# Optimization experiments

Hardware: AMD Instinct MI355X
Metric: run time of the kernel (lower is better)

The kernel has to match this reference:

```python
import jax, jax.numpy as jnp
import numpy as np

B = 1024      # graphs
NODES = 128   # nodes per graph (uniform -> batch_ptr = arange(B+1)*NODES)
IN = 64
HID = 256
OUT = 128
NBLK = 3
TAU = 0.25


def _ln(x, g, b):
    # LayerNorm over last dim, eps=1e-5 (torch default)
    mu = jnp.mean(x, axis=-1, keepdims=True)
    var = jnp.mean((x - mu) ** 2, axis=-1, keepdims=True)
    return (x - mu) / jnp.sqrt(var + 1e-5) * g + b


def setup_inputs() -> dict:
    key = jax.random.key(0)
    ks = jax.random.split(key, 4)
    sc = 0.05
    return {
        "H": jax.random.normal(ks[0], (B * NODES, IN), jnp.float32),
        "batch_ptr": jnp.arange(B + 1, dtype=jnp.int32) * NODES,
        # ResNetMLP params: stem Linear(IN->HID)+LN, NBLK residual blocks
        # Linear(HID->HID)+LN+ReLU, head Linear(HID->OUT)+LN (last_norm=True).
        "W_in": jax.random.normal(ks[1], (IN, HID), jnp.float32) * sc,
        "b_in": jnp.zeros((HID,), jnp.float32),
        "g_in": jnp.ones((HID,), jnp.float32),
        "beta_in": jnp.zeros((HID,), jnp.float32),
        "Wb": jax.random.normal(ks[2], (NBLK, HID, HID), jnp.float32) * sc,
        "bb": jnp.zeros((NBLK, HID), jnp.float32),
        "gb": jnp.ones((NBLK, HID), jnp.float32),
        "betab": jnp.zeros((NBLK, HID), jnp.float32),
        "W_out": jax.random.normal(ks[3], (HID, OUT), jnp.float32) * sc,
        "b_out": jnp.zeros((OUT,), jnp.float32),
        "g_out": jnp.ones((OUT,), jnp.float32),
        "beta_out": jnp.zeros((OUT,), jnp.float32),
    }


def reference(H, batch_ptr, W_in, b_in, g_in, beta_in, Wb, bb, gb, betab,
              W_out, b_out, g_out, beta_out):
    # ResNetMLP projection (dropout is identity in eval)
    x = jax.nn.relu(_ln(H @ W_in + b_in, g_in, beta_in))          # [N, HID]
    for k in range(NBLK):
        x = x + jax.nn.relu(_ln(x @ Wb[k] + bb[k], gb[k], betab[k]))
    z = _ln(x @ W_out + b_out, g_out, beta_out)                   # [N, OUT]

    # Uniform-size graphs: ragged per-graph loop vectorizes to [Bg, n, OUT]
    Bg = batch_ptr.shape[0] - 1
    n = H.shape[0] // Bg
    z3 = z.reshape(Bg, n, OUT)

    # s_i = mean_j ||z_i - z_j||_2 (includes j=i, distance 0)
    sq = jnp.sum(z3 * z3, axis=-1)                                # [Bg, n]
    d2 = sq[:, :, None] + sq[:, None, :] - 2.0 * jnp.einsum("bid,bjd->bij", z3, z3)
    d = jnp.sqrt(jnp.maximum(d2, 0.0) + 1e-12)                    # [Bg, n, n]
    s = jnp.mean(d, axis=-1)                                      # [Bg, n]

    w = jax.nn.softmax(s / TAU, axis=-1)                          # [Bg, n]
    v_loc = jnp.einsum("bi,bid->bd", w, z3)                       # [Bg, OUT]
    return v_loc, w
```

## Files before the change

kernel.cpp:

```cpp
#include <hip/hip_runtime.h>
#include <stdint.h>


typedef __attribute__((ext_vector_type(8))) short bf16x8;
typedef __attribute__((ext_vector_type(4))) float f32x4;

#define XB_STRIDE 264
#define YB_STRIDE 260
#define ZB_STRIDE 136
#define LDS_PAR   33280
#define LDS_TOTAL 36352

__device__ __forceinline__ unsigned int rne16(float f) {
  unsigned int u = __builtin_bit_cast(unsigned int, f);
  return u + 0x7fffu + ((u >> 16) & 1u);
}
__device__ __forceinline__ unsigned short f2bf(float f) {
  return (unsigned short)(rne16(f) >> 16);
}
__device__ __forceinline__ float bf2f(unsigned short h) {
  unsigned int u = ((unsigned int)h) << 16;
  return __builtin_bit_cast(float, u);
}
__device__ __forceinline__ f32x4 zero4() {
  f32x4 v; v.x = 0.f; v.y = 0.f; v.z = 0.f; v.w = 0.f; return v;
}
template <int CTRL>
__device__ __forceinline__ float dpp_add(float v) {
  int p = __builtin_amdgcn_update_dpp(0, __builtin_bit_cast(int, v),
                                      CTRL, 0xF, 0xF, true);
  return v + __builtin_bit_cast(float, p);
}
__device__ __forceinline__ float red16(float v) {
  v = dpp_add<0xB1>(v);
  v = dpp_add<0x4E>(v);
  v = dpp_add<0x141>(v);
  v = dpp_add<0x140>(v);
  return v;
}

__global__ void prep_weights(const float* __restrict__ Win, const float* __restrict__ Wb,
                             const float* __restrict__ Wout, unsigned short* __restrict__ ws) {
  int g = blockIdx.x * 256 + threadIdx.x;
  if (g >= 30720) return;
  const float* W; int N; int local;
  if (g < 2048) { W = Win; N = 256; local = g; }
  else if (g < 26624) {
    int i = g - 2048; int blk = i >> 13; local = i & 8191;
    W = Wb + blk * 65536; N = 256;
  } else { W = Wout; N = 128; local = g - 26624; }
  int f = local >> 6, lane = local & 63;
  int NTL = N >> 4;
  int kc = f / NTL, ntile = f - kc * NTL;
  int n = ntile * 16 + (lane & 15);
  int k0 = kc * 32 + (lane >> 4) * 8;
  unsigned short o[8];
#pragma unroll
  for (int e = 0; e < 8; ++e) o[e] = f2bf(W[(size_t)(k0 + e) * N + n]);
  *reinterpret_cast<uint4*>(ws + (size_t)g * 8) = *reinterpret_cast<uint4*>(o);
}

template <int KL, int N, int MODE>
__device__ __forceinline__ void layer(unsigned short* __restrict__ Xb,
                                      float* __restrict__ Yb, float* __restrict__ par,
                                      const unsigned short* __restrict__ Wf,
                                      int tid, int wave, int lane,
                                      const float* __restrict__ bias,
                                      const float* __restrict__ gam,
                                      const float* __restrict__ bet,
                                      float (&xprev)[16],
                                      unsigned short* __restrict__ Z, size_t rowglob) {
  constexpr int NT = N / 128;
  constexpr int NTL = N / 16;
  constexpr int KC = KL / 32;
  constexpr int J = N / 64;
  const int wc = wave;
  const int q = lane >> 4, l16 = lane & 15;
  const int colbase = wc * 16 * NT;
  const unsigned short* Wl = Wf + lane * 8;

  f32x4 acc[2][NT];
#pragma unroll
  for (int mt = 0; mt < 2; ++mt)
#pragma unroll
    for (int nt = 0; nt < NT; ++nt) acc[mt][nt] = zero4();

  bf16x8 bcur[NT];
#pragma unroll
  for (int nt = 0; nt < NT; ++nt)
    bcur[nt] = *reinterpret_cast<const bf16x8*>(Wl + (size_t)(wc * NT + nt) * 512);

  __syncthreads();
  for (int t = tid; t < 3 * N; t += 512) {
    float v = (t < N) ? bias[t] : (t < 2 * N) ? gam[t - N] : bet[t - 2 * N];
    par[t] = v;
  }
#pragma unroll
  for (int kc = 0; kc < KC; ++kc) {
    bf16x8 bnext[NT];
    if (kc + 1 < KC) {
#pragma unroll
      for (int nt = 0; nt < NT; ++nt)
        bnext[nt] = *reinterpret_cast<const bf16x8*>(
            Wl + (size_t)((kc + 1) * NTL + wc * NT + nt) * 512);
    }
    const int kk = kc * 32 + q * 8;
    bf16x8 a0 = *reinterpret_cast<const bf16x8*>(Xb + (l16) * XB_STRIDE + kk);
    bf16x8 a1 = *reinterpret_cast<const bf16x8*>(Xb + (16 + l16) * XB_STRIDE + kk);
#pragma unroll
    for (int nt = 0; nt < NT; ++nt)
      acc[0][nt] = __builtin_amdgcn_mfma_f32_16x16x32_bf16(a0, bcur[nt], acc[0][nt], 0, 0, 0);
#pragma unroll
    for (int nt = 0; nt < NT; ++nt)
      acc[1][nt] = __builtin_amdgcn_mfma_f32_16x16x32_bf16(a1, bcur[nt], acc[1][nt], 0, 0, 0);
    if (kc + 1 < KC) {
#pragma unroll
      for (int nt = 0; nt < NT; ++nt) bcur[nt] = bnext[nt];
    }
  }

  __syncthreads();

#pragma unroll
  for (int mt = 0; mt < 2; ++mt)
#pragma unroll
    for (int nt = 0; nt < NT; ++nt) {
      const int col = colbase + 16 * nt + l16;
#pragma unroll
      for (int r = 0; r < 4; ++r)
        Yb[(16 * mt + 4 * q + r) * YB_STRIDE + col] = acc[mt][nt][r];
    }
  __syncthreads();

  const int row = wave * 4 + q;
  const int cb = l16 * 4;
  float s1 = 0.f, s2 = 0.f;
#pragma unroll
  for (int j = 0; j < J; ++j) {
    f32x4 yv = *reinterpret_cast<const f32x4*>(Yb + row * YB_STRIDE + cb + 64 * j);
    f32x4 bv = *reinterpret_cast<const f32x4*>(par + cb + 64 * j);
#pragma unroll
    for (int i = 0; i < 4; ++i) {
      float t = yv[i] + bv[i];
      s1 += t; s2 = __builtin_fmaf(t, t, s2);
    }
  }
  s1 = red16(s1); s2 = red16(s2);
  const float mu = s1 * (1.0f / N);
  const float var = s2 * (1.0f / N) - mu * mu;
  const float rstd = rsqrtf(var + 1e-5f);
  const float nmr = -mu * rstd;
  unsigned int pkall[2 * J];
#pragma unroll
  for (int j = 0; j < J; ++j) {
    f32x4 yv = *reinterpret_cast<const f32x4*>(Yb + row * YB_STRIDE + cb + 64 * j);
    f32x4 bv = *reinterpret_cast<const f32x4*>(par + cb + 64 * j);
    f32x4 gv = *reinterpret_cast<const f32x4*>(par + N + cb + 64 * j);
    f32x4 ev = *reinterpret_cast<const f32x4*>(par + 2 * N + cb + 64 * j);
#pragma unroll
    for (int i = 0; i < 4; ++i) {
      const int e = 4 * j + i;
      float t = __builtin_fmaf(yv[i] + bv[i], rstd, nmr);
      float o = __builtin_fmaf(t, gv[i], ev[i]);
      float xv;
      if constexpr (MODE == 0) { xv = fmaxf(o, 0.f); xprev[e] = xv; }
      else if constexpr (MODE == 1) { xv = xprev[e] + fmaxf(o, 0.f); xprev[e] = xv; }
      else { xv = o; }
      if (i & 1)
        pkall[2 * j + (i >> 1)] = __builtin_amdgcn_perm(rne16(xv),
                       rne16(__builtin_bit_cast(float, pkall[2 * j + (i >> 1)])), 0x07060302);
      else
        pkall[2 * j + (i >> 1)] = __builtin_bit_cast(unsigned int, xv);
    }
  }
  if constexpr (MODE != 2) {
    __syncthreads();
    unsigned int* Xw = reinterpret_cast<unsigned int*>(Xb);
#pragma unroll
    for (int j = 0; j < J; ++j)
      *reinterpret_cast<uint2*>(Xw + row * 132 + 2 * l16 + 32 * j) =
          *reinterpret_cast<uint2*>(pkall + 2 * j);
  } else {
#pragma unroll
    for (int j = 0; j < J; ++j)
      *reinterpret_cast<uint2*>(Z + (rowglob + row) * 128 + cb + 64 * j) =
          *reinterpret_cast<uint2*>(pkall + 2 * j);
  }
}

__global__ __attribute__((amdgpu_flat_work_group_size(512, 512), amdgpu_waves_per_eu(6)))
void mlp_main(const float* __restrict__ H, const unsigned short* __restrict__ ws,
              const float* __restrict__ b_in, const float* __restrict__ g_in,
              const float* __restrict__ beta_in,
              const float* __restrict__ bb, const float* __restrict__ gb,
              const float* __restrict__ betab,
              const float* __restrict__ b_out, const float* __restrict__ g_out,
              const float* __restrict__ beta_out,
              unsigned short* __restrict__ Z) {
  extern __shared__ char smem[];
  unsigned short* Xb = (unsigned short*)smem;
  float* Yb = (float*)smem;
  float* par = (float*)(smem + LDS_PAR);
  const int tid = threadIdx.x;
  const int wave = tid >> 6, lane = tid & 63;
  const size_t rowglob = (size_t)blockIdx.x * 32;

  {
    int row = tid >> 4, c4 = (tid & 15) * 4;
    float4 f = *reinterpret_cast<const float4*>(H + (rowglob + row) * 64 + c4);
    uint2 o;
    o.x = __builtin_amdgcn_perm(rne16(f.y), rne16(f.x), 0x07060302);
    o.y = __builtin_amdgcn_perm(rne16(f.w), rne16(f.z), 0x07060302);
    *reinterpret_cast<uint2*>(Xb + row * XB_STRIDE + c4) = o;
  }

  float xprev[16];
  layer<64, 256, 0>(Xb, Yb, par, ws,           tid, wave, lane, b_in,     g_in,     beta_in,  xprev, Z, rowglob);
  layer<256, 256, 1>(Xb, Yb, par, ws + 16384,  tid, wave, lane, bb,       gb,       betab,    xprev, Z, rowglob);
  layer<256, 256, 1>(Xb, Yb, par, ws + 81920,  tid, wave, lane, bb + 256, gb + 256, betab + 256, xprev, Z, rowglob);
  layer<256, 256, 1>(Xb, Yb, par, ws + 147456, tid, wave, lane, bb + 512, gb + 512, betab + 512, xprev, Z, rowglob);
  layer<256, 128, 2>(Xb, Yb, par, ws + 212992, tid, wave, lane, b_out,    g_out,    beta_out, xprev, Z, rowglob);
}

__global__ __attribute__((amdgpu_flat_work_group_size(512, 512)))
void pool_main(const unsigned short* __restrict__ Z, float* __restrict__ out) {
  __shared__ unsigned short Zb[128 * ZB_STRIDE];
  __shared__ float sqv[128], sm[128], smw[128];
  const int tid = threadIdx.x;
  const int g = blockIdx.x;
  const int wave = tid >> 6, lane = tid & 63;
  const int q = lane >> 4, l16 = lane & 15;

  {
    int zr = tid >> 2, zc = (tid & 3) * 32;
    const uint4* zp = reinterpret_cast<const uint4*>(Z + ((size_t)g * 128 + zr) * 128 + zc);
    uint4* zd = reinterpret_cast<uint4*>(Zb + zr * ZB_STRIDE + zc);
    zd[0] = zp[0]; zd[1] = zp[1]; zd[2] = zp[2]; zd[3] = zp[3];
  }
  __syncthreads();

  f32x4 g2[8];
#pragma unroll
  for (int nt = 0; nt < 8; ++nt) g2[nt] = zero4();
#pragma unroll
  for (int ks = 0; ks < 4; ++ks) {
    int kk = ks * 32 + q * 8;
    bf16x8 a = *reinterpret_cast<const bf16x8*>(Zb + (16 * wave + l16) * ZB_STRIDE + kk);
#pragma unroll
    for (int nt = 0; nt < 8; ++nt) {
      bf16x8 bfr = *reinterpret_cast<const bf16x8*>(Zb + (16 * nt + l16) * ZB_STRIDE + kk);
      g2[nt] = __builtin_amdgcn_mfma_f32_16x16x32_bf16(a, bfr, g2[nt], 0, 0, 0);
    }
  }
  if ((l16 >> 2) == q) {
#pragma unroll
    for (int nt = 0; nt < 8; ++nt)
      if (nt == wave) {
#pragma unroll
        for (int r = 0; r < 4; ++r)
          if ((l16 & 3) == r) sqv[16 * wave + l16] = g2[nt][r];
      }
  }
  __syncthreads();
  float sqi[4];
#pragma unroll
  for (int r = 0; r < 4; ++r) sqi[r] = sqv[16 * wave + q * 4 + r];
  float sp[4] = {0.f, 0.f, 0.f, 0.f};
#pragma unroll
  for (int nt = 0; nt < 8; ++nt) {
    float sqj = sqv[16 * nt + l16];
#pragma unroll
    for (int r = 0; r < 4; ++r) {
      float d2 = sqi[r] + sqj - 2.0f * g2[nt][r];
      sp[r] += sqrtf(fmaxf(d2, 0.f) + 1e-12f);
    }
  }
#pragma unroll
  for (int d = 1; d < 16; d <<= 1) {
#pragma unroll
    for (int r = 0; r < 4; ++r) { float t = sp[r]; t += __shfl_xor(t, d); sp[r] = t; }
  }
  if (l16 == 0) {
#pragma unroll
    for (int r = 0; r < 4; ++r) sm[16 * wave + q * 4 + r] = sp[r] * (1.0f / 128.0f);
  }
  __syncthreads();
  if (wave == 0) {
    float l0 = sm[lane] * 4.0f;
    float l1 = sm[lane + 64] * 4.0f;
    float mx = fmaxf(l0, l1);
#pragma unroll
    for (int d = 1; d < 64; d <<= 1) mx = fmaxf(mx, __shfl_xor(mx, d));
    float e0 = __expf(l0 - mx), e1 = __expf(l1 - mx);
    float ss = e0 + e1;
#pragma unroll
    for (int d = 1; d < 64; d <<= 1) ss += __shfl_xor(ss, d);
    float inv = 1.0f / ss;
    float w0 = e0 * inv, w1 = e1 * inv;
    smw[lane] = w0;
    smw[lane + 64] = w1;
    out[131072 + g * 128 + lane] = w0;
    out[131072 + g * 128 + 64 + lane] = w1;
  }
  __syncthreads();
  {
    int c = 16 * wave + l16;
    float acv = 0.f;
#pragma unroll
    for (int i0 = 0; i0 < 32; ++i0) {
      int i = q * 32 + i0;
      acv += smw[i] * bf2f(Zb[i * ZB_STRIDE + c]);
    }
    acv += __shfl_xor(acv, 16);
    acv += __shfl_xor(acv, 32);
    if (q == 0) out[g * 128 + c] = acv;
  }
}

extern "C" void kernel_launch(void* const* d_in, const int* in_sizes, int n_in,
                              void* d_out, int out_size, void* d_ws, size_t ws_size,
                              hipStream_t stream) {
  (void)in_sizes; (void)n_in; (void)out_size; (void)ws_size;
  const float* H        = (const float*)d_in[0];
  const float* W_in     = (const float*)d_in[2];
  const float* b_in     = (const float*)d_in[3];
  const float* g_in     = (const float*)d_in[4];
  const float* beta_in  = (const float*)d_in[5];
  const float* Wb       = (const float*)d_in[6];
  const float* bb       = (const float*)d_in[7];
  const float* gb       = (const float*)d_in[8];
  const float* betab    = (const float*)d_in[9];
  const float* W_out    = (const float*)d_in[10];
  const float* b_out    = (const float*)d_in[11];
  const float* g_out    = (const float*)d_in[12];
  const float* beta_out = (const float*)d_in[13];
  float* out = (float*)d_out;
  unsigned short* ws = (unsigned short*)d_ws;
  unsigned short* Z = ws + 262144;

  prep_weights<<<120, 256, 0, stream>>>(W_in, Wb, W_out, ws);
  hipFuncSetAttribute(reinterpret_cast<const void*>(mlp_main),
                      hipFuncAttributeMaxDynamicSharedMemorySize, LDS_TOTAL);
  mlp_main<<<4096, 512, LDS_TOTAL, stream>>>(H, ws, b_in, g_in, beta_in,
                                             bb, gb, betab, b_out, g_out, beta_out, Z);
  pool_main<<<1024, 512, 0, stream>>>(Z, out);
}
```

Measured before the change: 225.5 us.

## Apply LayerNorm directly on MFMA accumulators with LDS atomic row statistics

Replaces the fp32 staging of the layer output through an LDS buffer with in-register bias, LayerNorm and ReLU on the MFMA accumulator fragments. Per-row sums and sums of squares are reduced with DPP inside each wave, then combined across waves with LDS atomics into small double-buffered arrays. Results are packed to bf16 using a DPP neighbour exchange and written straight into the next layer's input tile. This removes a full LDS round trip and one barrier per layer and roughly halves LDS use, which can raise occupancy, at the cost of LDS atomics and a different variance accumulation order.

```diff
diff --git a/kernel.cpp b/kernel.cpp
--- a/kernel.cpp
+++ b/kernel.cpp
@@ -6,10 +6,9 @@
 typedef __attribute__((ext_vector_type(4))) float f32x4;
 
 #define XB_STRIDE 264
-#define YB_STRIDE 260
 #define ZB_STRIDE 136
-#define LDS_PAR   33280
-#define LDS_TOTAL 36352
+#define LDS_PT    16896
+#define LDS_TOTAL 17408
 
 __device__ __forceinline__ unsigned int rne16(float f) {
   unsigned int u = __builtin_bit_cast(unsigned int, f);
@@ -30,6 +29,12 @@
   int p = __builtin_amdgcn_update_dpp(0, __builtin_bit_cast(int, v),
                                       CTRL, 0xF, 0xF, true);
   return v + __builtin_bit_cast(float, p);
+}
+template <int CTRL>
+__device__ __forceinline__ float dpp_mov(float v) {
+  int p = __builtin_amdgcn_update_dpp(0, __builtin_bit_cast(int, v),
+                                      CTRL, 0xF, 0xF, true);
+  return __builtin_bit_cast(float, p);
 }
 __device__ __forceinline__ float red16(float v) {
   v = dpp_add<0xB1>(v);
@@ -62,7 +67,7 @@
 
 template <int KL, int N, int MODE>
 __device__ __forceinline__ void layer(unsigned short* __restrict__ Xb,
-                                      float* __restrict__ Yb, float* __restrict__ par,
+                                      float* __restrict__ pt, float* __restrict__ ptn,
                                       const unsigned short* __restrict__ Wf,
                                       int tid, int wave, int lane,
                                       const float* __restrict__ bias,
@@ -73,12 +78,18 @@
   constexpr int NT = N / 128;
   constexpr int NTL = N / 16;
   constexpr int KC = KL / 32;
-  constexpr int J = N / 64;
   const int wc = wave;
   const int q = lane >> 4, l16 = lane & 15;
   const int colbase = wc * 16 * NT;
   const unsigned short* Wl = Wf + lane * 8;
 
+  float bv[NT], gv[NT], ev[NT];
+#pragma unroll
+  for (int nt = 0; nt < NT; ++nt) {
+    const int c = colbase + 16 * nt + l16;
+    bv[nt] = bias[c]; gv[nt] = gam[c]; ev[nt] = bet[c];
+  }
+
   f32x4 acc[2][NT];
 #pragma unroll
   for (int mt = 0; mt < 2; ++mt)
@@ -91,10 +102,6 @@
     bcur[nt] = *reinterpret_cast<const bf16x8*>(Wl + (size_t)(wc * NT + nt) * 512);
 
   __syncthreads();
-  for (int t = tid; t < 3 * N; t += 512) {
-    float v = (t < N) ? bias[t] : (t < 2 * N) ? gam[t - N] : bet[t - 2 * N];
-    par[t] = v;
-  }
 #pragma unroll
   for (int kc = 0; kc < KC; ++kc) {
     bf16x8 bnext[NT];
@@ -119,72 +126,87 @@
     }
   }
 
-  __syncthreads();
-
-#pragma unroll
-  for (int mt = 0; mt < 2; ++mt)
-#pragma unroll
-    for (int nt = 0; nt < NT; ++nt) {
-      const int col = colbase + 16 * nt + l16;
-#pragma unroll
-      for (int r = 0; r < 4; ++r)
-        Yb[(16 * mt + 4 * q + r) * YB_STRIDE + col] = acc[mt][nt][r];
-    }
-  __syncthreads();
-
-  const int row = wave * 4 + q;
-  const int cb = l16 * 4;
-  float s1 = 0.f, s2 = 0.f;
-#pragma unroll
-  for (int j = 0; j < J; ++j) {
-    f32x4 yv = *reinterpret_cast<const f32x4*>(Yb + row * YB_STRIDE + cb + 64 * j);
-    f32x4 bv = *reinterpret_cast<const f32x4*>(par + cb + 64 * j);
-#pragma unroll
-    for (int i = 0; i < 4; ++i) {
-      float t = yv[i] + bv[i];
-      s1 += t; s2 = __builtin_fmaf(t, t, s2);
-    }
-  }
-  s1 = red16(s1); s2 = red16(s2);
-  const float mu = s1 * (1.0f / N);
-  const float var = s2 * (1.0f / N) - mu * mu;
-  const float rstd = rsqrtf(var + 1e-5f);
-  const float nmr = -mu * rstd;
-  unsigned int pkall[2 * J];
-#pragma unroll
-  for (int j = 0; j < J; ++j) {
-    f32x4 yv = *reinterpret_cast<const f32x4*>(Yb + row * YB_STRIDE + cb + 64 * j);
-    f32x4 bv = *reinterpret_cast<const f32x4*>(par + cb + 64 * j);
-    f32x4 gv = *reinterpret_cast<const f32x4*>(par + N + cb + 64 * j);
-    f32x4 ev = *reinterpret_cast<const f32x4*>(par + 2 * N + cb + 64 * j);
-#pragma unroll
-    for (int i = 0; i < 4; ++i) {
-      const int e = 4 * j + i;
-      float t = __builtin_fmaf(yv[i] + bv[i], rstd, nmr);
-      float o = __builtin_fmaf(t, gv[i], ev[i]);
-      float xv;
-      if constexpr (MODE == 0) { xv = fmaxf(o, 0.f); xprev[e] = xv; }
-      else if constexpr (MODE == 1) { xv = xprev[e] + fmaxf(o, 0.f); xprev[e] = xv; }
-      else { xv = o; }
-      if (i & 1)
-        pkall[2 * j + (i >> 1)] = __builtin_amdgcn_perm(rne16(xv),
-                       rne16(__builtin_bit_cast(float, pkall[2 * j + (i >> 1)])), 0x07060302);
-      else
-        pkall[2 * j + (i >> 1)] = __builtin_bit_cast(unsigned int, xv);
-    }
-  }
-  if constexpr (MODE != 2) {
+  float s1p[2][4], s2p[2][4];
+#pragma unroll
+  for (int mt = 0; mt < 2; ++mt)
+#pragma unroll
+    for (int r = 0; r < 4; ++r) {
+      float a0 = acc[mt][0][r] + bv[0];
+      acc[mt][0][r] = a0;
+      float s1 = a0, s2 = a0 * a0;
+      if constexpr (NT == 2) {
+        float a1 = acc[mt][1][r] + bv[1];
+        acc[mt][1][r] = a1;
+        s1 += a1; s2 = __builtin_fmaf(a1, a1, s2);
+      }
+      s1p[mt][r] = red16(s1);
+      s2p[mt][r] = red16(s2);
+    }
+#pragma unroll
+  for (int mt = 0; mt < 2; ++mt)
+#pragma unroll
+    for (int r = 0; r < 4; ++r) {
+      if (l16 == mt * 4 + r) {
+        const int row = 16 * mt + 4 * q + r;
+        atomicAdd(&pt[row], s1p[mt][r]);
+        atomicAdd(&pt[32 + row], s2p[mt][r]);
+      }
+    }
+  __syncthreads();
+
+  f32x4 t1a = *reinterpret_cast<const f32x4*>(pt + 4 * q);
+  f32x4 t1b = *reinterpret_cast<const f32x4*>(pt + 16 + 4 * q);
+  f32x4 t2a = *reinterpret_cast<const f32x4*>(pt + 32 + 4 * q);
+  f32x4 t2b = *reinterpret_cast<const f32x4*>(pt + 48 + 4 * q);
+  if (tid < 64) ptn[tid] = 0.f;
+  constexpr float inv = 1.0f / N;
+  float rstd[2][4], nmr[2][4];
+#pragma unroll
+  for (int mt = 0; mt < 2; ++mt)
+#pragma unroll
+    for (int r = 0; r < 4; ++r) {
+      const float tt1 = mt ? t1b[r] : t1a[r];
+      const float tt2 = mt ? t2b[r] : t2a[r];
+      const float mu = tt1 * inv;
+      const float var = __builtin_fmaf(tt2, inv, -mu * mu);
+      const float rs = rsqrtf(var + 1e-5f);
+      rstd[mt][r] = rs; nmr[mt][r] = -mu * rs;
+    }
+
+  unsigned int* Xw = reinterpret_cast<unsigned int*>(Xb);
+#pragma unroll
+  for (int mt = 0; mt < 2; ++mt)
+#pragma unroll
+    for (int r = 0; r < 4; ++r) {
+      const int row = 16 * mt + 4 * q + r;
+      unsigned int ures[NT];
+#pragma unroll
+      for (int nt = 0; nt < NT; ++nt) {
+        const int e = mt * 8 + nt * 4 + r;
+        float t = __builtin_fmaf(acc[mt][nt][r], rstd[mt][r], nmr[mt][r]);
+        float o = __builtin_fmaf(t, gv[nt], ev[nt]);
+        float xv;
+        if constexpr (MODE == 0) { xv = fmaxf(o, 0.f); xprev[e] = xv; }
+        else if constexpr (MODE == 1) { xv = xprev[e] + fmaxf(o, 0.f); xprev[e] = xv; }
+        else { xv = o; (void)e; }
+        float pv = dpp_mov<0xB1>(xv);
+        float lo = (l16 & 1) ? pv : xv;
+        float hi = (l16 & 1) ? xv : pv;
+        ures[nt] = __builtin_amdgcn_perm(rne16(hi), rne16(lo), 0x07060302);
+      }
+      if constexpr (MODE != 2) {
+        const unsigned int u = (l16 & 1) ? ures[NT - 1] : ures[0];
+        const int idxu = 16 * wc + ((l16 & 1) ? 8 + (l16 >> 1) : (l16 >> 1));
+        Xw[row * 132 + idxu] = u;
+      } else {
+        if (!(l16 & 1)) Xw[row * 68 + 8 * wc + (l16 >> 1)] = ures[0];
+      }
+    }
+  if constexpr (MODE == 2) {
     __syncthreads();
-    unsigned int* Xw = reinterpret_cast<unsigned int*>(Xb);
-#pragma unroll
-    for (int j = 0; j < J; ++j)
-      *reinterpret_cast<uint2*>(Xw + row * 132 + 2 * l16 + 32 * j) =
-          *reinterpret_cast<uint2*>(pkall + 2 * j);
-  } else {
-#pragma unroll
-    for (int j = 0; j < J; ++j)
-      *reinterpret_cast<uint2*>(Z + (rowglob + row) * 128 + cb + 64 * j) =
-          *reinterpret_cast<uint2*>(pkall + 2 * j);
+    const int rr = tid >> 4, cc = (tid & 15) * 4;
+    uint4 v = *reinterpret_cast<const uint4*>(Xw + rr * 68 + cc);
+    *reinterpret_cast<uint4*>(Z + (rowglob + rr) * 128 + cc * 2) = v;
   }
 }
 
@@ -199,8 +221,7 @@
               unsigned short* __restrict__ Z) {
   extern __shared__ char smem[];
   unsigned short* Xb = (unsigned short*)smem;
-  float* Yb = (float*)smem;
-  float* par = (float*)(smem + LDS_PAR);
+  float* ptb = (float*)(smem + LDS_PT);
   const int tid = threadIdx.x;
   const int wave = tid >> 6, lane = tid & 63;
   const size_t rowglob = (size_t)blockIdx.x * 32;
@@ -212,14 +233,15 @@
     o.x = __builtin_amdgcn_perm(rne16(f.y), rne16(f.x), 0x07060302);
     o.y = __builtin_amdgcn_perm(rne16(f.w), rne16(f.z), 0x07060302);
     *reinterpret_cast<uint2*>(Xb + row * XB_STRIDE + c4) = o;
+    if (tid < 128) ptb[tid] = 0.f;
   }
 
   float xprev[16];
-  layer<64, 256, 0>(Xb, Yb, par, ws,           tid, wave, lane, b_in,     g_in,     beta_in,  xprev, Z, rowglob);
-  layer<256, 256, 1>(Xb, Yb, par, ws + 16384,  tid, wave, lane, bb,       gb,       betab,    xprev, Z, rowglob);
-  layer<256, 256, 1>(Xb, Yb, par, ws + 81920,  tid, wave, lane, bb + 256, gb + 256, betab + 256, xprev, Z, rowglob);
-  layer<256, 256, 1>(Xb, Yb, par, ws + 147456, tid, wave, lane, bb + 512, gb + 512, betab + 512, xprev, Z, rowglob);
-  layer<256, 128, 2>(Xb, Yb, par, ws + 212992, tid, wave, lane, b_out,    g_out,    beta_out, xprev, Z, rowglob);
+  layer<64, 256, 0>(Xb, ptb,      ptb + 64, ws,           tid, wave, lane, b_in,     g_in,     beta_in,     xprev, Z, rowglob);
+  layer<256, 256, 1>(Xb, ptb + 64, ptb,      ws + 16384,  tid, wave, lane, bb,       gb,       betab,       xprev, Z, rowglob);
+  layer<256, 256, 1>(Xb, ptb,      ptb + 64, ws + 81920,  tid, wave, lane, bb + 256, gb + 256, betab + 256, xprev, Z, rowglob);
+  layer<256, 256, 1>(Xb, ptb + 64, ptb,      ws + 147456, tid, wave, lane, bb + 512, gb + 512, betab + 512, xprev, Z, rowglob);
+  layer<256, 128, 2>(Xb, ptb,      ptb + 64, ws + 212992, tid, wave, lane, b_out,    g_out,    beta_out,    xprev, Z, rowglob);
 }
 
 __global__ __attribute__((amdgpu_flat_work_group_size(512, 512)))
@@ -339,8 +361,6 @@
   unsigned short* Z = ws + 262144;
 
   prep_weights<<<120, 256, 0, stream>>>(W_in, Wb, W_out, ws);
-  hipFuncSetAttribute(reinterpret_cast<const void*>(mlp_main),
-                      hipFuncAttributeMaxDynamicSharedMemorySize, LDS_TOTAL);
   mlp_main<<<4096, 512, LDS_TOTAL, stream>>>(H, ws, b_in, g_in, beta_in,
                                              bb, gb, betab, b_out, g_out, beta_out, Z);
   pool_main<<<1024, 512, 0, stream>>>(Z, out);
```

Measured after the change: 294.5 us. 1.31x slower.

## Double MLP row tile to 64 rows per block for weight reuse

Applied to the files above, without the earlier changes.

Each mlp_main block now handles 64 rows instead of 32, running four M-tiles of MFMAs for every weight fragment loaded from global memory. This halves the total weight traffic and the number of blocks, and doubles the accumulator and residual register state. The LDS footprint roughly doubles and the waves-per-EU hint drops from 6 to 4, so fewer blocks fit per CU and latency hiding may suffer.

```diff
diff --git a/kernel.cpp b/kernel.cpp
--- a/kernel.cpp
+++ b/kernel.cpp
@@ -8,8 +8,8 @@
 #define XB_STRIDE 264
 #define YB_STRIDE 260
 #define ZB_STRIDE 136
-#define LDS_PAR   33280
-#define LDS_TOTAL 36352
+#define LDS_PAR   66560
+#define LDS_TOTAL 69632
 
 __device__ __forceinline__ unsigned int rne16(float f) {
   unsigned int u = __builtin_bit_cast(unsigned int, f);
@@ -68,7 +68,7 @@
                                       const float* __restrict__ bias,
                                       const float* __restrict__ gam,
                                       const float* __restrict__ bet,
-                                      float (&xprev)[16],
+                                      float (&xprev)[32],
                                       unsigned short* __restrict__ Z, size_t rowglob) {
   constexpr int NT = N / 128;
   constexpr int NTL = N / 16;
@@ -79,9 +79,9 @@
   const int colbase = wc * 16 * NT;
   const unsigned short* Wl = Wf + lane * 8;
 
-  f32x4 acc[2][NT];
-#pragma unroll
-  for (int mt = 0; mt < 2; ++mt)
+  f32x4 acc[4][NT];
+#pragma unroll
+  for (int mt = 0; mt < 4; ++mt)
 #pragma unroll
     for (int nt = 0; nt < NT; ++nt) acc[mt][nt] = zero4();
 
@@ -105,14 +105,13 @@
             Wl + (size_t)((kc + 1) * NTL + wc * NT + nt) * 512);
     }
     const int kk = kc * 32 + q * 8;
-    bf16x8 a0 = *reinterpret_cast<const bf16x8*>(Xb + (l16) * XB_STRIDE + kk);
-    bf16x8 a1 = *reinterpret_cast<const bf16x8*>(Xb + (16 + l16) * XB_STRIDE + kk);
-#pragma unroll
-    for (int nt = 0; nt < NT; ++nt)
-      acc[0][nt] = __builtin_amdgcn_mfma_f32_16x16x32_bf16(a0, bcur[nt], acc[0][nt], 0, 0, 0);
-#pragma unroll
-    for (int nt = 0; nt < NT; ++nt)
-      acc[1][nt] = __builtin_amdgcn_mfma_f32_16x16x32_bf16(a1, bcur[nt], acc[1][nt], 0, 0, 0);
+#pragma unroll
+    for (int mt = 0; mt < 4; ++mt) {
+      bf16x8 a = *reinterpret_cast<const bf16x8*>(Xb + (16 * mt + l16) * XB_STRIDE + kk);
+#pragma unroll
+      for (int nt = 0; nt < NT; ++nt)
+        acc[mt][nt] = __builtin_amdgcn_mfma_f32_16x16x32_bf16(a, bcur[nt], acc[mt][nt], 0, 0, 0);
+    }
     if (kc + 1 < KC) {
 #pragma unroll
       for (int nt = 0; nt < NT; ++nt) bcur[nt] = bnext[nt];
@@ -122,7 +121,7 @@
   __syncthreads();
 
 #pragma unroll
-  for (int mt = 0; mt < 2; ++mt)
+  for (int mt = 0; mt < 4; ++mt)
 #pragma unroll
     for (int nt = 0; nt < NT; ++nt) {
       const int col = colbase + 16 * nt + l16;
@@ -132,63 +131,71 @@
     }
   __syncthreads();
 
-  const int row = wave * 4 + q;
   const int cb = l16 * 4;
-  float s1 = 0.f, s2 = 0.f;
-#pragma unroll
-  for (int j = 0; j < J; ++j) {
-    f32x4 yv = *reinterpret_cast<const f32x4*>(Yb + row * YB_STRIDE + cb + 64 * j);
-    f32x4 bv = *reinterpret_cast<const f32x4*>(par + cb + 64 * j);
-#pragma unroll
-    for (int i = 0; i < 4; ++i) {
-      float t = yv[i] + bv[i];
-      s1 += t; s2 = __builtin_fmaf(t, t, s2);
-    }
-  }
-  s1 = red16(s1); s2 = red16(s2);
-  const float mu = s1 * (1.0f / N);
-  const float var = s2 * (1.0f / N) - mu * mu;
-  const float rstd = rsqrtf(var + 1e-5f);
-  const float nmr = -mu * rstd;
-  unsigned int pkall[2 * J];
-#pragma unroll
-  for (int j = 0; j < J; ++j) {
-    f32x4 yv = *reinterpret_cast<const f32x4*>(Yb + row * YB_STRIDE + cb + 64 * j);
-    f32x4 bv = *reinterpret_cast<const f32x4*>(par + cb + 64 * j);
-    f32x4 gv = *reinterpret_cast<const f32x4*>(par + N + cb + 64 * j);
-    f32x4 ev = *reinterpret_cast<const f32x4*>(par + 2 * N + cb + 64 * j);
-#pragma unroll
-    for (int i = 0; i < 4; ++i) {
-      const int e = 4 * j + i;
-      float t = __builtin_fmaf(yv[i] + bv[i], rstd, nmr);
-      float o = __builtin_fmaf(t, gv[i], ev[i]);
-      float xv;
-      if constexpr (MODE == 0) { xv = fmaxf(o, 0.f); xprev[e] = xv; }
-      else if constexpr (MODE == 1) { xv = xprev[e] + fmaxf(o, 0.f); xprev[e] = xv; }
-      else { xv = o; }
-      if (i & 1)
-        pkall[2 * j + (i >> 1)] = __builtin_amdgcn_perm(rne16(xv),
-                       rne16(__builtin_bit_cast(float, pkall[2 * j + (i >> 1)])), 0x07060302);
-      else
-        pkall[2 * j + (i >> 1)] = __builtin_bit_cast(unsigned int, xv);
+  unsigned int pk[2][2 * J];
+#pragma unroll
+  for (int h = 0; h < 2; ++h) {
+    const int row = 32 * h + wave * 4 + q;
+    float s1 = 0.f, s2 = 0.f;
+#pragma unroll
+    for (int j = 0; j < J; ++j) {
+      f32x4 yv = *reinterpret_cast<const f32x4*>(Yb + row * YB_STRIDE + cb + 64 * j);
+      f32x4 bv = *reinterpret_cast<const f32x4*>(par + cb + 64 * j);
+#pragma unroll
+      for (int i = 0; i < 4; ++i) {
+        float t = yv[i] + bv[i];
+        s1 += t; s2 = __builtin_fmaf(t, t, s2);
+      }
+    }
+    s1 = red16(s1); s2 = red16(s2);
+    const float mu = s1 * (1.0f / N);
+    const float var = s2 * (1.0f / N) - mu * mu;
+    const float rstd = rsqrtf(var + 1e-5f);
+    const float nmr = -mu * rstd;
+#pragma unroll
+    for (int j = 0; j < J; ++j) {
+      f32x4 yv = *reinterpret_cast<const f32x4*>(Yb + row * YB_STRIDE + cb + 64 * j);
+      f32x4 bv = *reinterpret_cast<const f32x4*>(par + cb + 64 * j);
+      f32x4 gv = *reinterpret_cast<const f32x4*>(par + N + cb + 64 * j);
+      f32x4 ev = *reinterpret_cast<const f32x4*>(par + 2 * N + cb + 64 * j);
+#pragma unroll
+      for (int i = 0; i < 4; ++i) {
+        const int e = 16 * h + 4 * j + i;
+        float t = __builtin_fmaf(yv[i] + bv[i], rstd, nmr);
+        float o = __builtin_fmaf(t, gv[i], ev[i]);
+        float xv;
+        if constexpr (MODE == 0) { xv = fmaxf(o, 0.f); xprev[e] = xv; }
+        else if constexpr (MODE == 1) { xv = xprev[e] + fmaxf(o, 0.f); xprev[e] = xv; }
+        else { xv = o; (void)e; }
+        if (i & 1)
+          pk[h][2 * j + (i >> 1)] = __builtin_amdgcn_perm(rne16(xv),
+                         rne16(__builtin_bit_cast(float, pk[h][2 * j + (i >> 1)])), 0x07060302);
+        else
+          pk[h][2 * j + (i >> 1)] = __builtin_bit_cast(unsigned int, xv);
+      }
+    }
+    if constexpr (MODE == 2) {
+#pragma unroll
+      for (int j = 0; j < J; ++j)
+        *reinterpret_cast<uint2*>(Z + (rowglob + row) * 128 + cb + 64 * j) =
+            *reinterpret_cast<uint2*>(&pk[h][2 * j]);
     }
   }
   if constexpr (MODE != 2) {
     __syncthreads();
     unsigned int* Xw = reinterpret_cast<unsigned int*>(Xb);
 #pragma unroll
-    for (int j = 0; j < J; ++j)
-      *reinterpret_cast<uint2*>(Xw + row * 132 + 2 * l16 + 32 * j) =
-          *reinterpret_cast<uint2*>(pkall + 2 * j);
-  } else {
-#pragma unroll
-    for (int j = 0; j < J; ++j)
-      *reinterpret_cast<uint2*>(Z + (rowglob + row) * 128 + cb + 64 * j) =
-          *reinterpret_cast<uint2*>(pkall + 2 * j);
-  }
-}
-
-__global__ __attribute__((amdgpu_flat_work_group_size(512, 512), amdgpu_waves_per_eu(6)))
+    for (int h = 0; h < 2; ++h) {
+      const int row = 32 * h + wave * 4 + q;
+#pragma unroll
+      for (int j = 0; j < J; ++j)
+        *reinterpret_cast<uint2*>(Xw + row * 132 + 2 * l16 + 32 * j) =
+            *reinterpret_cast<uint2*>(&pk[h][2 * j]);
+    }
+  }
+}
+
+__global__ __attribute__((amdgpu_flat_work_group_size(512, 512), amdgpu_waves_per_eu(4)))
 void mlp_main(const float* __restrict__ H, const unsigned short* __restrict__ ws,
               const float* __restrict__ b_in, const float* __restrict__ g_in,
               const float* __restrict__ beta_in,
@@ -203,23 +210,27 @@
   float* par = (float*)(smem + LDS_PAR);
   const int tid = threadIdx.x;
   const int wave = tid >> 6, lane = tid & 63;
-  const size_t rowglob = (size_t)blockIdx.x * 32;
+  const size_t rowglob = (size_t)blockIdx.x * 64;
 
   {
-    int row = tid >> 4, c4 = (tid & 15) * 4;
-    float4 f = *reinterpret_cast<const float4*>(H + (rowglob + row) * 64 + c4);
-    uint2 o;
-    o.x = __builtin_amdgcn_perm(rne16(f.y), rne16(f.x), 0x07060302);
-    o.y = __builtin_amdgcn_perm(rne16(f.w), rne16(f.z), 0x07060302);
-    *reinterpret_cast<uint2*>(Xb + row * XB_STRIDE + c4) = o;
-  }
-
-  float xprev[16];
-  layer<64, 256, 0>(Xb, Yb, par, ws,           tid, wave, lane, b_in,     g_in,     beta_in,  xprev, Z, rowglob);
-  layer<256, 256, 1>(Xb, Yb, par, ws + 16384,  tid, wave, lane, bb,       gb,       betab,    xprev, Z, rowglob);
+    int row = tid >> 3, c8 = (tid & 7) * 8;
+    const float* hp = H + (rowglob + row) * 64 + c8;
+    float4 f0 = *reinterpret_cast<const float4*>(hp);
+    float4 f1 = *reinterpret_cast<const float4*>(hp + 4);
+    uint4 o;
+    o.x = __builtin_amdgcn_perm(rne16(f0.y), rne16(f0.x), 0x07060302);
+    o.y = __builtin_amdgcn_perm(rne16(f0.w), rne16(f0.z), 0x07060302);
+    o.z = __builtin_amdgcn_perm(rne16(f1.y), rne16(f1.x), 0x07060302);
+    o.w = __builtin_amdgcn_perm(rne16(f1.w), rne16(f1.z), 0x07060302);
+    *reinterpret_cast<uint4*>(Xb + row * XB_STRIDE + c8) = o;
+  }
+
+  float xprev[32];
+  layer<64, 256, 0>(Xb, Yb, par, ws,           tid, wave, lane, b_in,     g_in,     beta_in,     xprev, Z, rowglob);
+  layer<256, 256, 1>(Xb, Yb, par, ws + 16384,  tid, wave, lane, bb,       gb,       betab,       xprev, Z, rowglob);
   layer<256, 256, 1>(Xb, Yb, par, ws + 81920,  tid, wave, lane, bb + 256, gb + 256, betab + 256, xprev, Z, rowglob);
   layer<256, 256, 1>(Xb, Yb, par, ws + 147456, tid, wave, lane, bb + 512, gb + 512, betab + 512, xprev, Z, rowglob);
-  layer<256, 128, 2>(Xb, Yb, par, ws + 212992, tid, wave, lane, b_out,    g_out,    beta_out, xprev, Z, rowglob);
+  layer<256, 128, 2>(Xb, Yb, par, ws + 212992, tid, wave, lane, b_out,    g_out,    beta_out,    xprev, Z, rowglob);
 }
 
 __global__ __attribute__((amdgpu_flat_work_group_size(512, 512)))
@@ -341,7 +352,7 @@
   prep_weights<<<120, 256, 0, stream>>>(W_in, Wb, W_out, ws);
   hipFuncSetAttribute(reinterpret_cast<const void*>(mlp_main),
                       hipFuncAttributeMaxDynamicSharedMemorySize, LDS_TOTAL);
-  mlp_main<<<4096, 512, LDS_TOTAL, stream>>>(H, ws, b_in, g_in, beta_in,
+  mlp_main<<<2048, 512, LDS_TOTAL, stream>>>(H, ws, b_in, g_in, beta_in,
                                              bb, gb, betab, b_out, g_out, beta_out, Z);
   pool_main<<<1024, 512, 0, stream>>>(Z, out);
 }
```

New measurement: 209.7 us. 1.08x faster.
